# Kernel optimization log

Hardware: AMD Instinct MI355X
Metric: run time of the kernel (lower is better)

## Reference

```python
import jax, jax.numpy as jnp
import numpy as np

BS, L, NPH, NQ, H = 64, 512, 16, 16, 1024
EPS = 1e-5

def _ln(x, g, b):
    m = jnp.mean(x, axis=-1, keepdims=True)
    v = jnp.mean((x - m) ** 2, axis=-1, keepdims=True)
    return (x - m) * jax.lax.rsqrt(v + EPS) * g + b

def setup_inputs() -> dict:
    key = jax.random.key(0)
    ks = jax.random.split(key, 24)
    s = 0.02
    inp = {
        "lang_context_feat": jax.random.normal(ks[0], (BS, L, H), jnp.float32),
        "lang_query_feat": jax.random.normal(ks[1], (BS, NPH, H), jnp.float32),
        "mask_query_context": jax.random.randint(ks[2], (BS, NPH, L), 0, 2).astype(bool),
        "query_embed": jax.random.normal(ks[3], (NQ, 2 * H), jnp.float32) * s,
        # linear1/2/3: hidden -> hidden (stored [in, out])
        "W1": jax.random.normal(ks[4], (H, H), jnp.float32) * s, "b1": jnp.zeros((H,), jnp.float32),
        "W2": jax.random.normal(ks[5], (H, H), jnp.float32) * s, "b2": jnp.zeros((H,), jnp.float32),
        "W3": jax.random.normal(ks[6], (H, H), jnp.float32) * s, "b3": jnp.zeros((H,), jnp.float32),
        # context_out: Linear(h,h) + LayerNorm(h)
        "Wc": jax.random.normal(ks[7], (H, H), jnp.float32) * s, "bc": jnp.zeros((H,), jnp.float32),
        "gc": jnp.ones((H,), jnp.float32), "betac": jnp.zeros((H,), jnp.float32),
        # fuse_encoder_query: Linear(2h,h)+LN+ReLU+Dropout(eval)+Linear(h,h)+LN+ReLU
        "Wf1": jax.random.normal(ks[8], (2 * H, H), jnp.float32) * s, "bf1": jnp.zeros((H,), jnp.float32),
        "gf1": jnp.ones((H,), jnp.float32), "betaf1": jnp.zeros((H,), jnp.float32),
        "Wf2": jax.random.normal(ks[9], (H, H), jnp.float32) * s, "bf2": jnp.zeros((H,), jnp.float32),
        "gf2": jnp.ones((H,), jnp.float32), "betaf2": jnp.zeros((H,), jnp.float32),
    }
    return inp

def reference(lang_context_feat, lang_query_feat, mask_query_context,
              query_embed, W1, b1, W2, b2, W3, b3,
              Wc, bc, gc, betac,
              Wf1, bf1, gf1, betaf1, Wf2, bf2, gf2, betaf2):
    # single-query attention: k from first context token, q/v from all tokens
    k = lang_context_feat[:, 0:1, :] @ W1 + b1          # [bs,1,h]
    q = lang_context_feat @ W2 + b2                     # [bs,L,h]
    v = lang_context_feat @ W3 + b3                     # [bs,L,h]
    att = jnp.einsum("bih,blh->bil", k, q)             # [bs,1,L]
    att = jnp.broadcast_to(att, mask_query_context.shape)  # [bs,n_ph,L]
    att = jnp.where(mask_query_context, -jnp.inf, att)
    p = jax.nn.softmax(att, axis=-1)                    # [bs,n_ph,L]
    ctx = jnp.einsum("bpl,blh->bph", p, v)             # [bs,n_ph,h]
    ctx = _ln(ctx @ Wc + bc, gc, betac)
    ctx = lang_context_feat[:, None, 0, :] + ctx        # residual with first token
    x = jnp.concatenate([ctx, lang_query_feat], axis=-1)   # [bs,n_ph,2h]
    x = jax.nn.relu(_ln(x @ Wf1 + bf1, gf1, betaf1))        # dropout: eval mode (identity)
    x = jax.nn.relu(_ln(x @ Wf2 + bf2, gf2, betaf2))        # [bs,n_ph,h]
    # repeat(1,1,1,2) on last dim == tile [x, x]
    pq = jnp.concatenate([x, x], axis=-1)[:, :, None, :]    # [bs,n_ph,1,2h]
    pq = pq + query_embed[None, None, :, :]                 # [bs,n_ph,n_q,2h]
    pq = pq.reshape(pq.shape[0], -1, 2 * H).transpose(1, 0, 2)  # [n_ph*n_q,bs,2h]
    return pq[..., :H], pq[..., H:]
```

## Files before the change

### kernel.cpp

```cpp
#include <hip/hip_runtime.h>

typedef __bf16 bf16;
typedef __bf16 bf16x8 __attribute__((ext_vector_type(8)));
typedef __bf16 bf16x4 __attribute__((ext_vector_type(4)));
typedef float f32x4 __attribute__((ext_vector_type(4)));

#define LCTX 512
#define HD 1024

__device__ __forceinline__ float wave_sum(float v) {
    for (int off = 32; off; off >>= 1) v += __shfl_xor(v, off, 64);
    return v;
}
__device__ __forceinline__ float wave_max(float v) {
    for (int off = 32; off; off >>= 1) v = fmaxf(v, __shfl_xor(v, off, 64));
    return v;
}

__global__ __launch_bounds__(256) void prep_kernel(const float* __restrict__ W3,
                                                   const float* __restrict__ Wc,
                                                   const float* __restrict__ Wf1,
                                                   const float* __restrict__ Wf2,
                                                   const float* __restrict__ lq,
                                                   const float* __restrict__ x,
                                                   const float* __restrict__ W1,
                                                   bf16* __restrict__ W3t, bf16* __restrict__ Wct,
                                                   bf16* __restrict__ Wf1t, bf16* __restrict__ Wf2t,
                                                   bf16* __restrict__ X,
                                                   float* __restrict__ kpartial) {
    __shared__ __align__(16) char smem[33792];
    int blk = blockIdx.x, t = threadIdx.x;
    if (blk < 5120) {
        float (*tile)[33] = (float(*)[33])smem;
        const float* W; bf16* Wt; int K, N, i;
        if (blk < 1024)      { W = W3;  Wt = W3t;  K = 1024; N = 1024; i = blk; }
        else if (blk < 2048) { W = Wc;  Wt = Wct;  K = 1024; N = 1024; i = blk - 1024; }
        else if (blk < 3072) { W = Wf2; Wt = Wf2t; K = 1024; N = 1024; i = blk - 2048; }
        else                 { W = Wf1; Wt = Wf1t; K = 2048; N = 1024; i = blk - 3072; }
        int k0 = (i >> 5) * 32, n0 = (i & 31) * 32;
        int c = t & 31, r = t >> 5;
#pragma unroll
        for (int j = 0; j < 4; j++)
            tile[r + j * 8][c] = W[(size_t)(k0 + r + j * 8) * N + n0 + c];
        __syncthreads();
#pragma unroll
        for (int j = 0; j < 4; j++)
            Wt[(size_t)(n0 + r + j * 8) * K + k0 + c] = (bf16)tile[c][r + j * 8];
    } else if (blk < 6144) {
        int i = (blk - 5120) * 256 + t;
        float4 v = ((const float4*)lq)[i];
        int row = i >> 8, h4 = i & 255;
        bf16x4 o = {(bf16)v.x, (bf16)v.y, (bf16)v.z, (bf16)v.w};
        *(bf16x4*)(X + (size_t)row * 2048 + 1024 + h4 * 4) = o;
    } else {
        float (*xs)[68] = (float(*)[68])smem;
        float (*wsm)[64] = (float(*)[64])(smem + 17408);
        int kv = blk - 6144;
        int n0 = (kv & 15) * 64, k0 = (kv >> 4) * 64;
#pragma unroll
        for (int i = 0; i < 4; i++) {
            int f = t + i * 256;
            int b = f >> 4, c = f & 15;
            *(float4*)&xs[b][c * 4] =
                *(const float4*)(x + (size_t)b * LCTX * HD + k0 + c * 4);
        }
#pragma unroll
        for (int i = 0; i < 4; i++) {
            int f = t + i * 256;
            int r = f >> 4, c = f & 15;
            *(float4*)&wsm[r][c * 4] =
                *(const float4*)(W1 + (size_t)(k0 + r) * 1024 + n0 + c * 4);
        }
        __syncthreads();
        int tb = t >> 4, tc = t & 15;
        int b0 = tb * 4;
        float acc[4][4] = {};
        for (int kk = 0; kk < 64; kk += 4) {
            float4 w0 = *(const float4*)&wsm[kk + 0][tc * 4];
            float4 w1 = *(const float4*)&wsm[kk + 1][tc * 4];
            float4 w2 = *(const float4*)&wsm[kk + 2][tc * 4];
            float4 w3 = *(const float4*)&wsm[kk + 3][tc * 4];
            float4 xv[4];
#pragma unroll
            for (int bi = 0; bi < 4; bi++) xv[bi] = *(const float4*)&xs[b0 + bi][kk];
#pragma unroll
            for (int bi = 0; bi < 4; bi++) {
                acc[bi][0] += xv[bi].x * w0.x + xv[bi].y * w1.x + xv[bi].z * w2.x + xv[bi].w * w3.x;
                acc[bi][1] += xv[bi].x * w0.y + xv[bi].y * w1.y + xv[bi].z * w2.y + xv[bi].w * w3.y;
                acc[bi][2] += xv[bi].x * w0.z + xv[bi].y * w1.z + xv[bi].z * w2.z + xv[bi].w * w3.z;
                acc[bi][3] += xv[bi].x * w0.w + xv[bi].y * w1.w + xv[bi].z * w2.w + xv[bi].w * w3.w;
            }
        }
        float* pout = kpartial + ((size_t)(kv >> 4) * 64 + b0) * 1024 + n0 + tc * 4;
#pragma unroll
        for (int bi = 0; bi < 4; bi++)
            *(float4*)(pout + (size_t)bi * 1024) =
                make_float4(acc[bi][0], acc[bi][1], acc[bi][2], acc[bi][3]);
    }
}

__global__ __launch_bounds__(256) void mmat_kernel(const float* __restrict__ partial,
                                                   const float* __restrict__ b1,
                                                   const float* __restrict__ W2,
                                                   float* __restrict__ mout) {
    __shared__ float ks[1024];
    int b = blockIdx.x, i0 = blockIdx.y * 64, t = threadIdx.x;
    {
        float4 acc = ((const float4*)b1)[t];
#pragma unroll
        for (int kt = 0; kt < 16; kt++) {
            float4 v = ((const float4*)(partial + ((size_t)kt * 64 + b) * 1024))[t];
            acc.x += v.x; acc.y += v.y; acc.z += v.z; acc.w += v.w;
        }
        *(float4*)&ks[t * 4] = acc;
    }
    __syncthreads();
    int wave = t >> 6, lane = t & 63;
    for (int rr = 0; rr < 16; rr++) {
        int i = i0 + wave * 16 + rr;
        const float* wrow = W2 + (size_t)i * 1024;
        float s = 0.f;
#pragma unroll
        for (int j = 0; j < 4; j++) {
            float4 wv = ((const float4*)wrow)[lane + j * 64];
            const float4 kv = *(const float4*)&ks[(lane + j * 64) * 4];
            s += wv.x * kv.x + wv.y * kv.y + wv.z * kv.z + wv.w * kv.w;
        }
        s = wave_sum(s);
        if (lane == 0) mout[(size_t)b * 1024 + i] = s;
    }
}

__global__ __launch_bounds__(256) void att_kernel(const float* __restrict__ x,
                                                  const float* __restrict__ m,
                                                  float* __restrict__ att) {
    __shared__ float ms[1024];
    int b = blockIdx.x, l0 = blockIdx.y * 32, t = threadIdx.x;
    *(float4*)&ms[t * 4] = ((const float4*)(m + (size_t)b * 1024))[t];
    __syncthreads();
    int wave = t >> 6, lane = t & 63;
    for (int rr = 0; rr < 8; rr++) {
        int l = l0 + wave * 8 + rr;
        const float* xr = x + ((size_t)b * LCTX + l) * HD;
        float s = 0.f;
#pragma unroll
        for (int j = 0; j < 4; j++) {
            float4 xv = ((const float4*)xr)[lane + j * 64];
            const float4 mv = *(const float4*)&ms[(lane + j * 64) * 4];
            s += xv.x * mv.x + xv.y * mv.y + xv.z * mv.z + xv.w * mv.w;
        }
        s = wave_sum(s);
        if (lane == 0) att[(size_t)b * LCTX + l] = s;
    }
}

__global__ __launch_bounds__(256) void ysm_kernel(const float* __restrict__ att,
                                                  const unsigned char* __restrict__ mask,
                                                  const float* __restrict__ x,
                                                  bf16* __restrict__ y) {
    __shared__ float ps[16][512];
    __shared__ float att_s[512];
    __shared__ int sstr;
    int b = blockIdx.x, c0 = blockIdx.y * 256, t = threadIdx.x;
    int wave = t >> 6, lane = t & 63;
    if (t == 0) sstr = 4;
    if (t < 128) ((float4*)att_s)[t] = ((const float4*)(att + (size_t)b * LCTX))[t];
    __syncthreads();
    if (t < 128 && ((const unsigned int*)mask)[t] > 1u) sstr = 1;
    __syncthreads();
    int stride = sstr;
#pragma unroll
    for (int q = 0; q < 4; q++) {
        int pp = wave * 4 + q;
        size_t mbase = ((size_t)(b * 16 + pp)) * LCTX;
        float av[8];
#pragma unroll
        for (int j = 0; j < 8; j++) {
            int l = lane + j * 64;
            bool mk = mask[(mbase + l) * (size_t)stride] != 0;
            av[j] = mk ? -1e30f : att_s[l];
        }
        float mx = av[0];
#pragma unroll
        for (int j = 1; j < 8; j++) mx = fmaxf(mx, av[j]);
        mx = wave_max(mx);
        float s = 0.f;
#pragma unroll
        for (int j = 0; j < 8; j++) {
            av[j] = (av[j] <= -1e29f) ? 0.f : expf(av[j] - mx);
            s += av[j];
        }
        s = wave_sum(s);
        float inv = 1.f / s;
#pragma unroll
        for (int j = 0; j < 8; j++) ps[pp][lane + j * 64] = av[j] * inv;
    }
    __syncthreads();
    float acc[16] = {};
    const float* xb = x + (size_t)b * LCTX * HD + c0 + t;
    for (int l = 0; l < 512; l++) {
        float xv = xb[(size_t)l * HD];
#pragma unroll
        for (int q = 0; q < 16; q++) acc[q] += ps[q][l] * xv;
    }
#pragma unroll
    for (int q = 0; q < 16; q++)
        y[((size_t)(b * 16 + q)) * HD + c0 + t] = (bf16)acc[q];
}

__device__ __forceinline__ void gl16(const bf16* g, bf16* l) {
    __builtin_amdgcn_global_load_lds((const __attribute__((address_space(1))) void*)g,
                                     (__attribute__((address_space(3))) void*)l, 16, 0, 0);
}
__device__ __forceinline__ bf16x8 ldsfrag(const bf16* base, int row, int kb) {
    return *(const bf16x8*)(base + row * 64 + ((kb ^ (row & 7)) << 3));
}

template <bool OUT_BF16>
__global__ __launch_bounds__(256) void gemm_kernel(const bf16* __restrict__ A, int lda,
                                                   const bf16* __restrict__ Bt, int ldb,
                                                   const float* __restrict__ bias,
                                                   void* __restrict__ Cv, int ldc, int K) {
    __shared__ bf16 sA[2][4096];
    __shared__ bf16 sB[2][4096];
    int tid = threadIdx.x;
    int wave = tid >> 6, lane = tid & 63;
    int m0 = blockIdx.x * 64, n0 = blockIdx.y * 64;
    int wr = (wave >> 1) * 32, wc = (wave & 1) * 32;
    int l16 = lane & 15, lhi = lane >> 4;
    int r0 = tid >> 3, kb = tid & 7;
    int r1 = r0 + 32;
    int sk0 = (kb ^ (r0 & 7)) << 3;
    int sk1 = (kb ^ (r1 & 7)) << 3;
    const bf16* A0 = A + (size_t)(m0 + r0) * lda + sk0;
    const bf16* A1 = A + (size_t)(m0 + r1) * lda + sk1;
    const bf16* B0 = Bt + (size_t)(n0 + r0) * ldb + sk0;
    const bf16* B1 = Bt + (size_t)(n0 + r1) * ldb + sk1;
    int wb0 = (wave * 64) * 8;
    int wb1 = (256 + wave * 64) * 8;

    f32x4 acc00 = {}, acc01 = {}, acc10 = {}, acc11 = {};

    int nt = K >> 6;
    gl16(A0, &sA[0][wb0]); gl16(A1, &sA[0][wb1]);
    gl16(B0, &sB[0][wb0]); gl16(B1, &sB[0][wb1]);
    asm volatile("s_waitcnt vmcnt(0)" ::: "memory");
    __syncthreads();
    int cur = 0;
    for (int tI = 0; tI < nt; ++tI) {
        if (tI + 1 < nt) {
            int ko = (tI + 1) << 6;
            gl16(A0 + ko, &sA[cur ^ 1][wb0]); gl16(A1 + ko, &sA[cur ^ 1][wb1]);
            gl16(B0 + ko, &sB[cur ^ 1][wb0]); gl16(B1 + ko, &sB[cur ^ 1][wb1]);
        }
        const bf16* a = sA[cur];
        const bf16* bt = sB[cur];
#pragma unroll
        for (int ks = 0; ks < 2; ks++) {
            int kbb = ks * 4 + lhi;
            bf16x8 a0 = ldsfrag(a, wr + l16, kbb);
            bf16x8 a1v = ldsfrag(a, wr + 16 + l16, kbb);
            bf16x8 b0v = ldsfrag(bt, wc + l16, kbb);
            bf16x8 b1v = ldsfrag(bt, wc + 16 + l16, kbb);
            acc00 = __builtin_amdgcn_mfma_f32_16x16x32_bf16(a0, b0v, acc00, 0, 0, 0);
            acc01 = __builtin_amdgcn_mfma_f32_16x16x32_bf16(a0, b1v, acc01, 0, 0, 0);
            acc10 = __builtin_amdgcn_mfma_f32_16x16x32_bf16(a1v, b0v, acc10, 0, 0, 0);
            acc11 = __builtin_amdgcn_mfma_f32_16x16x32_bf16(a1v, b1v, acc11, 0, 0, 0);
        }
        asm volatile("s_waitcnt vmcnt(0)" ::: "memory");
        __syncthreads();
        cur ^= 1;
    }
    f32x4 accs[2][2] = {{acc00, acc01}, {acc10, acc11}};
#pragma unroll
    for (int mi = 0; mi < 2; mi++)
#pragma unroll
        for (int ni = 0; ni < 2; ni++)
#pragma unroll
            for (int r = 0; r < 4; r++) {
                int row = m0 + wr + mi * 16 + lhi * 4 + r;
                int col = n0 + wc + ni * 16 + l16;
                float v = accs[mi][ni][r] + bias[col];
                if (OUT_BF16)
                    ((bf16*)Cv)[(size_t)row * ldc + col] = (bf16)v;
                else
                    ((float*)Cv)[(size_t)row * ldc + col] = v;
            }
}

template <int MODE>
__global__ __launch_bounds__(256) void ln_kernel(const float* __restrict__ C,
                                                 const float* __restrict__ g,
                                                 const float* __restrict__ beta,
                                                 const float* __restrict__ resid,
                                                 void* __restrict__ out) {
    __shared__ float r1[8], r2[8];
    int row = blockIdx.x, t = threadIdx.x;
    float4 v = ((const float4*)(C + (size_t)row * 1024))[t];
    float s = v.x + v.y + v.z + v.w;
    float s2 = v.x * v.x + v.y * v.y + v.z * v.z + v.w * v.w;
    s = wave_sum(s); s2 = wave_sum(s2);
    int wave = t >> 6, lane = t & 63;
    if (lane == 0) { r1[wave] = s; r2[wave] = s2; }
    __syncthreads();
    float S = r1[0] + r1[1] + r1[2] + r1[3];
    float S2 = r2[0] + r2[1] + r2[2] + r2[3];
    float mean = S * (1.f / 1024.f);
    float var = S2 * (1.f / 1024.f) - mean * mean;
    float inv = rsqrtf(var + 1e-5f);
    float4 gv = ((const float4*)g)[t];
    float4 bv = ((const float4*)beta)[t];
    float o[4];
    o[0] = (v.x - mean) * inv * gv.x + bv.x;
    o[1] = (v.y - mean) * inv * gv.y + bv.y;
    o[2] = (v.z - mean) * inv * gv.z + bv.z;
    o[3] = (v.w - mean) * inv * gv.w + bv.w;
    if (MODE == 0) {
        int b = row >> 4;
        const float* x0 = resid + (size_t)b * LCTX * HD + t * 4;
        bf16x4 w = {(bf16)(o[0] + x0[0]), (bf16)(o[1] + x0[1]),
                    (bf16)(o[2] + x0[2]), (bf16)(o[3] + x0[3])};
        *(bf16x4*)((bf16*)out + (size_t)row * 2048 + t * 4) = w;
    } else {
        bf16x4 w = {(bf16)fmaxf(o[0], 0.f), (bf16)fmaxf(o[1], 0.f),
                    (bf16)fmaxf(o[2], 0.f), (bf16)fmaxf(o[3], 0.f)};
        *(bf16x4*)((bf16*)out + (size_t)row * 1024 + t * 4) = w;
    }
}

__global__ __launch_bounds__(256) void lnout_kernel(const float* __restrict__ C,
                                                    const float* __restrict__ g,
                                                    const float* __restrict__ beta,
                                                    const float* __restrict__ qe,
                                                    float* __restrict__ out) {
    __shared__ float r1[8], r2[8];
    int row = blockIdx.x, t = threadIdx.x;
    int b = row >> 4, pp = row & 15;
    float4 v = ((const float4*)(C + (size_t)row * 1024))[t];
    float s = v.x + v.y + v.z + v.w;
    float s2 = v.x * v.x + v.y * v.y + v.z * v.z + v.w * v.w;
    s = wave_sum(s); s2 = wave_sum(s2);
    int wave = t >> 6, lane = t & 63;
    if (lane == 0) { r1[wave] = s; r2[wave] = s2; }
    __syncthreads();
    float S = r1[0] + r1[1] + r1[2] + r1[3];
    float S2 = r2[0] + r2[1] + r2[2] + r2[3];
    float mean = S * (1.f / 1024.f);
    float var = S2 * (1.f / 1024.f) - mean * mean;
    float inv = rsqrtf(var + 1e-5f);
    float4 gv = ((const float4*)g)[t];
    float4 bv = ((const float4*)beta)[t];
    float4 ov;
    ov.x = fmaxf((v.x - mean) * inv * gv.x + bv.x, 0.f);
    ov.y = fmaxf((v.y - mean) * inv * gv.y + bv.y, 0.f);
    ov.z = fmaxf((v.z - mean) * inv * gv.z + bv.z, 0.f);
    ov.w = fmaxf((v.w - mean) * inv * gv.w + bv.w, 0.f);
    float* out0 = out;
    float* out1 = out + (size_t)256 * 64 * 1024;
#pragma unroll
    for (int q = 0; q < 16; q++) {
        float4 q0 = ((const float4*)(qe + (size_t)q * 2048))[t];
        float4 q1 = ((const float4*)(qe + (size_t)q * 2048 + 1024))[t];
        size_t orow = ((size_t)(pp * 16 + q) * 64 + b) * 1024;
        ((float4*)(out0 + orow))[t] =
            make_float4(ov.x + q0.x, ov.y + q0.y, ov.z + q0.z, ov.w + q0.w);
        ((float4*)(out1 + orow))[t] =
            make_float4(ov.x + q1.x, ov.y + q1.y, ov.z + q1.z, ov.w + q1.w);
    }
}

extern "C" void kernel_launch(void* const* d_in, const int* in_sizes, int n_in,
                              void* d_out, int out_size, void* d_ws, size_t ws_size,
                              hipStream_t stream) {
    const float* x      = (const float*)d_in[0];
    const float* lq     = (const float*)d_in[1];
    const unsigned char* mask = (const unsigned char*)d_in[2];
    const float* qe     = (const float*)d_in[3];
    const float* W1     = (const float*)d_in[4];
    const float* b1     = (const float*)d_in[5];
    const float* W2     = (const float*)d_in[6];
    const float* W3     = (const float*)d_in[8];
    const float* b3     = (const float*)d_in[9];
    const float* Wc     = (const float*)d_in[10];
    const float* bc     = (const float*)d_in[11];
    const float* gc     = (const float*)d_in[12];
    const float* betac  = (const float*)d_in[13];
    const float* Wf1    = (const float*)d_in[14];
    const float* bf1    = (const float*)d_in[15];
    const float* gf1    = (const float*)d_in[16];
    const float* betaf1 = (const float*)d_in[17];
    const float* Wf2    = (const float*)d_in[18];
    const float* bf2    = (const float*)d_in[19];
    const float* gf2    = (const float*)d_in[20];
    const float* betaf2 = (const float*)d_in[21];

    char* ws = (char*)d_ws;
    const size_t MB = 1 << 20;
    bf16* W3t   = (bf16*)(ws + 0 * MB);
    bf16* Wct   = (bf16*)(ws + 2 * MB);
    bf16* Wf1t  = (bf16*)(ws + 4 * MB);
    bf16* Wf2t  = (bf16*)(ws + 8 * MB);
    bf16* X     = (bf16*)(ws + 10 * MB);
    float* mbuf = (float*)(ws + 14 * MB + 256 * 1024);
    float* attb = (float*)(ws + 14 * MB + 512 * 1024);
    bf16* ybuf  = (bf16*)(ws + 17 * MB);
    bf16* ctxp  = (bf16*)(ws + 19 * MB);
    float* Cbuf = (float*)(ws + 21 * MB);
    bf16* t1    = (bf16*)(ws + 25 * MB);
    float* kpartial = Cbuf;

    prep_kernel<<<6400, 256, 0, stream>>>(W3, Wc, Wf1, Wf2, lq, x, W1,
                                          W3t, Wct, Wf1t, Wf2t, X, kpartial);
    mmat_kernel<<<dim3(64, 16), 256, 0, stream>>>(kpartial, b1, W2, mbuf);
    att_kernel<<<dim3(64, 16), 256, 0, stream>>>(x, mbuf, attb);
    ysm_kernel<<<dim3(64, 4), 256, 0, stream>>>(attb, mask, x, ybuf);
    gemm_kernel<true><<<dim3(16, 16), 256, 0, stream>>>(ybuf, 1024, W3t, 1024, b3,
                                                        ctxp, 1024, 1024);
    gemm_kernel<false><<<dim3(16, 16), 256, 0, stream>>>(ctxp, 1024, Wct, 1024, bc,
                                                         Cbuf, 1024, 1024);
    ln_kernel<0><<<1024, 256, 0, stream>>>(Cbuf, gc, betac, x, X);
    gemm_kernel<false><<<dim3(16, 16), 256, 0, stream>>>(X, 2048, Wf1t, 2048, bf1,
                                                         Cbuf, 1024, 2048);
    ln_kernel<1><<<1024, 256, 0, stream>>>(Cbuf, gf1, betaf1, nullptr, t1);
    gemm_kernel<false><<<dim3(16, 16), 256, 0, stream>>>(t1, 1024, Wf2t, 1024, bf2,
                                                         Cbuf, 1024, 1024);
    lnout_kernel<<<1024, 256, 0, stream>>>(Cbuf, gf2, betaf2, qe, (float*)d_out);
}
```

Measured before the change: 257.7 us.

## Split softmax-weighted context sum over sequence chunks with separate reduction

The probability-weighted sum over context tokens changes from splitting the hidden dimension across blocks to splitting the 512 sequence positions into four chunks. Each block covers all 1024 hidden columns with float4 loads and writes fp32 partial sums, and a new reduction kernel adds the four partials and converts them to bf16. This gives wider, more coalesced loads and a shorter serial loop per thread. The cost is a 16 MB partial buffer that must be written and read back, one extra kernel launch, 64 accumulator registers per thread, and a softmax recomputed redundantly in every block.

```diff
diff --git a/kernel.cpp b/kernel.cpp
--- a/kernel.cpp
+++ b/kernel.cpp
@@ -154,14 +154,15 @@
     }
 }
 
-__global__ __launch_bounds__(256) void ysm_kernel(const float* __restrict__ att,
-                                                  const unsigned char* __restrict__ mask,
-                                                  const float* __restrict__ x,
-                                                  bf16* __restrict__ y) {
-    __shared__ float ps[16][512];
+__global__ __launch_bounds__(256) void ypart_kernel(const float* __restrict__ att,
+                                                    const unsigned char* __restrict__ mask,
+                                                    const float* __restrict__ x,
+                                                    float* __restrict__ ypartial) {
+    __shared__ float ps[16][128];
     __shared__ float att_s[512];
     __shared__ int sstr;
-    int b = blockIdx.x, c0 = blockIdx.y * 256, t = threadIdx.x;
+    int b = blockIdx.x, lqi = blockIdx.y, t = threadIdx.x;
+    int l0 = lqi * 128;
     int wave = t >> 6, lane = t & 63;
     if (t == 0) sstr = 4;
     if (t < 128) ((float4*)att_s)[t] = ((const float4*)(att + (size_t)b * LCTX))[t];
@@ -193,19 +194,44 @@
         s = wave_sum(s);
         float inv = 1.f / s;
 #pragma unroll
-        for (int j = 0; j < 8; j++) ps[pp][lane + j * 64] = av[j] * inv;
-    }
-    __syncthreads();
-    float acc[16] = {};
-    const float* xb = x + (size_t)b * LCTX * HD + c0 + t;
-    for (int l = 0; l < 512; l++) {
-        float xv = xb[(size_t)l * HD];
-#pragma unroll
-        for (int q = 0; q < 16; q++) acc[q] += ps[q][l] * xv;
-    }
+        for (int j = 0; j < 8; j++) {
+            int l = lane + j * 64;
+            if (l >= l0 && l < l0 + 128) ps[pp][l - l0] = av[j] * inv;
+        }
+    }
+    __syncthreads();
+    float4 acc[16];
+#pragma unroll
+    for (int q = 0; q < 16; q++) acc[q] = make_float4(0.f, 0.f, 0.f, 0.f);
+    const float4* xb = (const float4*)(x + ((size_t)b * LCTX + l0) * HD) + t;
+    for (int l = 0; l < 128; l++) {
+        float4 xv = xb[(size_t)l * 256];
+#pragma unroll
+        for (int q = 0; q < 16; q++) {
+            float pv = ps[q][l];
+            acc[q].x += pv * xv.x; acc[q].y += pv * xv.y;
+            acc[q].z += pv * xv.z; acc[q].w += pv * xv.w;
+        }
+    }
+    float* yp = ypartial + ((size_t)lqi * 1024 + b * 16) * 1024 + t * 4;
 #pragma unroll
     for (int q = 0; q < 16; q++)
-        y[((size_t)(b * 16 + q)) * HD + c0 + t] = (bf16)acc[q];
+        *(float4*)(yp + (size_t)q * 1024) = acc[q];
+}
+
+__global__ __launch_bounds__(256) void yred_kernel(const float* __restrict__ ypartial,
+                                                   bf16* __restrict__ y) {
+    int i = blockIdx.x * 256 + threadIdx.x;
+    float4 a0 = ((const float4*)ypartial)[i];
+    float4 a1 = ((const float4*)(ypartial + (size_t)1 * 1024 * 1024))[i];
+    float4 a2 = ((const float4*)(ypartial + (size_t)2 * 1024 * 1024))[i];
+    float4 a3 = ((const float4*)(ypartial + (size_t)3 * 1024 * 1024))[i];
+    float sx = a0.x + a1.x + a2.x + a3.x;
+    float sy = a0.y + a1.y + a2.y + a3.y;
+    float sz = a0.z + a1.z + a2.z + a3.z;
+    float sw = a0.w + a1.w + a2.w + a3.w;
+    bf16x4 o = {(bf16)sx, (bf16)sy, (bf16)sz, (bf16)sw};
+    *(bf16x4*)(y + (size_t)i * 4) = o;
 }
 
 __device__ __forceinline__ void gl16(const bf16* g, bf16* l) {
@@ -407,13 +433,15 @@
     bf16* ctxp  = (bf16*)(ws + 19 * MB);
     float* Cbuf = (float*)(ws + 21 * MB);
     bf16* t1    = (bf16*)(ws + 25 * MB);
+    float* ypartial = (float*)(ws + 32 * MB);
     float* kpartial = Cbuf;
 
     prep_kernel<<<6400, 256, 0, stream>>>(W3, Wc, Wf1, Wf2, lq, x, W1,
                                           W3t, Wct, Wf1t, Wf2t, X, kpartial);
     mmat_kernel<<<dim3(64, 16), 256, 0, stream>>>(kpartial, b1, W2, mbuf);
     att_kernel<<<dim3(64, 16), 256, 0, stream>>>(x, mbuf, attb);
-    ysm_kernel<<<dim3(64, 4), 256, 0, stream>>>(attb, mask, x, ybuf);
+    ypart_kernel<<<dim3(64, 4), 256, 0, stream>>>(attb, mask, x, ypartial);
+    yred_kernel<<<1024, 256, 0, stream>>>(ypartial, ybuf);
     gemm_kernel<true><<<dim3(16, 16), 256, 0, stream>>>(ybuf, 1024, W3t, 1024, b3,
                                                         ctxp, 1024, 1024);
     gemm_kernel<false><<<dim3(16, 16), 256, 0, stream>>>(ctxp, 1024, Wct, 1024, bc,
```

Result: faster. 241.3 us (-6.3%).
